# Kernel optimization log

Hardware: AMD Instinct MI355X
Metric: run time of the kernel (lower is better)

## Reference

```python
import jax, jax.numpy as jnp
import numpy as np
from jax import lax

C, K, EMB = 10, 32, 32
B, H, W = 32, 128, 128
DIRS = ((-1, 0), (1, 0), (0, -1), (0, 1))  # up, down, left, right


def _shift(x, dh, dw):
    # shift (B,H,W,...) by (dh,dw) with zero fill; x[b,h,w] <- x[b,h+dh,w+dw]
    pad = [(0, 0), (max(dh, 0), max(-dh, 0)), (max(dw, 0), max(-dw, 0))] + [(0, 0)] * (x.ndim - 3)
    xp = jnp.pad(x, pad)
    h0, w0 = max(-dh, 0), max(-dw, 0)
    return lax.dynamic_slice_in_dim(lax.dynamic_slice_in_dim(xp, h0, x.shape[1], 1), w0, x.shape[2], 2)


def conv(x, w, b):
    y = lax.conv_general_dilated(x, w, (1, 1), 'SAME',
                                 dimension_numbers=('NHWC', 'HWIO', 'NHWC'))
    return y + b


def small_cnn(x, w1, b1, w2, b2, w3, b3):
    x = jax.nn.relu(conv(x, w1, b1))
    x = jax.nn.relu(conv(x, w2, b2))
    return conv(x, w3, b3)


def neighbor_affinity(phi, tau=0.5):
    # phi: (B,H,W,D) -> w: (B,H,W,4) Gaussian feature affinity to 4 neighbors
    ones = jnp.ones(phi.shape[:3] + (1,), phi.dtype)
    ws = []
    for dh, dw in DIRS:
        nb = _shift(phi, dh, dw)
        valid = _shift(ones, dh, dw)[..., 0]
        d2 = jnp.sum((phi - nb) ** 2, axis=-1)
        ws.append(jnp.exp(-d2 / tau) * valid)
    return jnp.stack(ws, axis=-1)


def init_seeds_soft(Bv, Hv, Wv, Kv, dtype=jnp.float32):
    # K seeds on a gh x gw grid; soft assignment by squared distance
    gh = 4
    gw = Kv // gh
    sh = (jnp.arange(gh, dtype=dtype) + 0.5) * (Hv / gh)
    sw = (jnp.arange(gw, dtype=dtype) + 0.5) * (Wv / gw)
    seed_h = jnp.repeat(sh, gw)  # (K,)
    seed_w = jnp.tile(sw, gh)    # (K,)
    hh = jnp.arange(Hv, dtype=dtype)[:, None, None]
    ww = jnp.arange(Wv, dtype=dtype)[None, :, None]
    d2 = (hh - seed_h) ** 2 + (ww - seed_w) ** 2  # (H,W,K)
    sigma2 = (Hv / gh) * (Wv / gw)
    A = jax.nn.softmax(-d2 / sigma2, axis=-1)
    return jnp.broadcast_to(A[None], (Bv, Hv, Wv, Kv))


def soft_message_pass(A, w, beta=2.0):
    # aggregate neighbor assignments weighted by affinity, renormalize over K
    agg = jnp.zeros_like(A)
    for d, (dh, dw) in enumerate(DIRS):
        agg = agg + w[..., d:d + 1] * _shift(A, dh, dw)
    return jax.nn.softmax(beta * agg, axis=-1)


def soft_pool_features(G, A):
    # G:(B,H,W,C), A:(B,H,W,K) -> T:(B,K,1+2+C+4)
    Bv, Hv, Wv, Cv = G.shape
    eps = 1e-6
    mass = jnp.sum(A, axis=(1, 2)) + eps                      # (B,K)
    hh = (jnp.arange(Hv, dtype=G.dtype) + 0.5) / Hv
    ww = (jnp.arange(Wv, dtype=G.dtype) + 0.5) / Wv
    h_c = jnp.einsum('bhwk,h->bk', A, hh) / mass
    w_c = jnp.einsum('bhwk,w->bk', A, ww) / mass
    col = jnp.einsum('bhwk,bhwc->bkc', A, G) / mass[..., None]
    h2 = jnp.einsum('bhwk,h->bk', A, hh ** 2) / mass
    w2 = jnp.einsum('bhwk,w->bk', A, ww ** 2) / mass
    h_sd = jnp.sqrt(jax.nn.relu(h2 - h_c ** 2) + eps)
    w_sd = jnp.sqrt(jax.nn.relu(w2 - w_c ** 2) + eps)
    size = (mass / (Hv * Wv))[..., None]                      # (B,K,1)
    cen = jnp.stack([h_c, w_c], axis=-1)                      # (B,K,2)
    bbox = jnp.stack([h_c - h_sd, h_c + h_sd, w_c - w_sd, w_c + w_sd], axis=-1)
    return jnp.concatenate([size, cen, col, bbox], axis=-1)


def setup_inputs() -> dict:
    key = jax.random.key(0)
    ks = jax.random.split(key, 4)
    X = jax.random.randint(ks[0], (B, H, W), 0, C)
    w1 = jax.random.normal(ks[1], (3, 3, C, 32), jnp.float32) * (1.0 / np.sqrt(9 * C))
    w2 = jax.random.normal(ks[2], (3, 3, 32, 32), jnp.float32) * (1.0 / np.sqrt(9 * 32))
    w3 = jax.random.normal(ks[3], (1, 1, 32, EMB), jnp.float32) * (1.0 / np.sqrt(32))
    return {'X': X, 'w1': w1, 'b1': jnp.zeros((32,), jnp.float32),
            'w2': w2, 'b2': jnp.zeros((32,), jnp.float32),
            'w3': w3, 'b3': jnp.zeros((EMB,), jnp.float32)}


def reference(X, w1, b1, w2, b2, w3, b3):
    G = jax.nn.one_hot(X, C, dtype=jnp.float32)              # (B,H,W,C)
    phi = small_cnn(G, w1, b1, w2, b2, w3, b3)               # (B,H,W,EMB)
    w = neighbor_affinity(phi)                               # (B,H,W,4)
    A = init_seeds_soft(G.shape[0], G.shape[1], G.shape[2], K, G.dtype)
    for _ in range(8):
        A = soft_message_pass(A, w, beta=2.0)
    T = soft_pool_features(G, A)
    return A, T
```

## Files before the change

### kernel.cpp

```cpp
#include <hip/hip_runtime.h>
#include <math.h>

#define HD 128
#define WD 128
#define BB 32
#define KK 32
#define NPIX (BB*HD*WD)

typedef _Float16 f16;
typedef __attribute__((ext_vector_type(8))) _Float16 f16x8;
typedef __attribute__((ext_vector_type(4))) float f32x4;

__device__ __forceinline__ int swz(int row, int g){
  return row*64 + (((g + (row >> 1)) & 3) << 4);
}

__global__ __launch_bounds__(512, 2) void cnn_kernel(
    const int* __restrict__ X,
    const float* __restrict__ w1, const float* __restrict__ b1,
    const float* __restrict__ w2, const float* __restrict__ b2,
    const float* __restrict__ w3, const float* __restrict__ b3,
    f16* __restrict__ phi)
{
  __shared__ f16 sW1f[9*11*40];
  __shared__ int   sX[20*36];
  __shared__ float sB2[32], sB3[32];
  __shared__ f16 x1[612*32];
  __shared__ f16 w2t[9*32*32];
  __shared__ f16 w3t[32*32];

  const int tid = threadIdx.x;
  const int img = blockIdx.z;
  const int bh0 = blockIdx.y * 16;
  const int bw0 = blockIdx.x * 32;

  for (int i = tid; i < 9*11*32; i += 512) {
    int tap = i / 352, c = (i % 352) >> 5, oc = i & 31;
    float v = (c < 10) ? w1[tap*320 + c*32 + oc] : 0.f;
    if (tap == 4 && c < 10) v += b1[oc];
    sW1f[(tap*11 + c)*40 + oc] = (f16)v;
  }
  for (int i = tid; i < 9*32*32; i += 512) {
    int tap = i >> 10, ic = (i >> 5) & 31, oc = i & 31;
    int off = swz(tap*32 + oc, ic >> 3) + (ic & 7)*2;
    *(f16*)((char*)w2t + off) = (f16)w2[i];
  }
  for (int i = tid; i < 32*32; i += 512) {
    int ic = i >> 5, oe = i & 31;
    int off = swz(oe, ic >> 3) + (ic & 7)*2;
    *(f16*)((char*)w3t + off) = (f16)w3[i];
  }
  if (tid < 32) { sB2[tid] = b2[tid]; sB3[tid] = b3[tid]; }
  for (int i = tid; i < 20*36; i += 512) {
    int ti = i / 36, tj = i % 36;
    int gh = bh0 - 2 + ti, gw = bw0 - 2 + tj;
    sX[i] = (gh >= 0 && gh < HD && gw >= 0 && gw < WD) ? X[(img*HD + gh)*WD + gw] : 10;
  }
  __syncthreads();

  for (int p = tid; p < 612; p += 512) {
    int hr = p / 34, hc = p - hr*34;
    int gh = bh0 + hr - 1, gw = bw0 + hc - 1;
    if (gh >= 0 && gh < HD && gw >= 0 && gw < WD) {
      f16x8 acc[4];
      {
        int c = sX[hr*36 + hc];
        const f16* wr = &sW1f[c*40];
        #pragma unroll
        for (int g = 0; g < 4; g++) acc[g] = *(const f16x8*)(wr + g*8);
      }
      #pragma unroll
      for (int tap = 1; tap < 9; tap++) {
        const int ti = tap/3, tj = tap%3;
        int c = sX[(hr+ti)*36 + hc + tj];
        const f16* wr = &sW1f[(tap*11 + c)*40];
        #pragma unroll
        for (int g = 0; g < 4; g++) acc[g] += *(const f16x8*)(wr + g*8);
      }
      f16x8 z;
      #pragma unroll
      for (int j = 0; j < 8; j++) z[j] = (f16)0.f;
      #pragma unroll
      for (int g = 0; g < 4; g++) {
        f16x8 r = acc[g];
        #pragma unroll
        for (int j = 0; j < 8; j++) r[j] = (r[j] > (f16)0.f) ? r[j] : (f16)0.f;
        *(f16x8*)((char*)x1 + swz(p, g)) = r;
      }
    } else {
      f16x8 z;
      #pragma unroll
      for (int j = 0; j < 8; j++) z[j] = (f16)0.f;
      #pragma unroll
      for (int g = 0; g < 4; g++) *(f16x8*)((char*)x1 + swz(p, g)) = z;
    }
  }
  __syncthreads();

  const int lane = tid & 63;
  const int wv   = tid >> 6;
  const int lr   = lane & 15;
  const int kg   = lane >> 4;
  const int mts  = wv * 4;

  int arow0[4];
  #pragma unroll
  for (int q = 0; q < 4; q++) {
    int px = (mts + q)*16 + lr;
    arow0[q] = (px >> 5)*34 + (px & 31);
  }
  float b2v0 = sB2[lr], b2v1 = sB2[lr + 16];
  f32x4 acc[4][2];
  #pragma unroll
  for (int q = 0; q < 4; q++) {
    acc[q][0] = (f32x4){b2v0, b2v0, b2v0, b2v0};
    acc[q][1] = (f32x4){b2v1, b2v1, b2v1, b2v1};
  }
  #pragma unroll
  for (int tap = 0; tap < 9; tap++) {
    const int ti = tap/3, tj = tap%3;
    f16x8 bf0 = *(const f16x8*)((const char*)w2t + swz(tap*32 + lr,      kg));
    f16x8 bf1 = *(const f16x8*)((const char*)w2t + swz(tap*32 + lr + 16, kg));
    #pragma unroll
    for (int q = 0; q < 4; q++) {
      int row = arow0[q] + ti*34 + tj;
      f16x8 af = *(const f16x8*)((const char*)x1 + swz(row, kg));
      acc[q][0] = __builtin_amdgcn_mfma_f32_16x16x32_f16(af, bf0, acc[q][0], 0, 0, 0);
      acc[q][1] = __builtin_amdgcn_mfma_f32_16x16x32_f16(af, bf1, acc[q][1], 0, 0, 0);
    }
  }
  __syncthreads();

  #pragma unroll
  for (int q = 0; q < 4; q++)
    #pragma unroll
    for (int nt = 0; nt < 2; nt++) {
      int oc = nt*16 + lr;
      #pragma unroll
      for (int rg = 0; rg < 4; rg++) {
        int px = (mts + q)*16 + kg*4 + rg;
        int off = swz(px, oc >> 3) + (oc & 7)*2;
        *(f16*)((char*)x1 + off) = (f16)fmaxf(acc[q][nt][rg], 0.f);
      }
    }
  __syncthreads();

  {
    f16x8 cf0 = *(const f16x8*)((const char*)w3t + swz(lr,      kg));
    f16x8 cf1 = *(const f16x8*)((const char*)w3t + swz(lr + 16, kg));
    float b3v0 = sB3[lr], b3v1 = sB3[lr + 16];
    #pragma unroll
    for (int q = 0; q < 4; q++) {
      f16x8 af = *(const f16x8*)((const char*)x1 + swz((mts + q)*16 + lr, kg));
      f32x4 o0 = (f32x4){b3v0, b3v0, b3v0, b3v0};
      f32x4 o1 = (f32x4){b3v1, b3v1, b3v1, b3v1};
      o0 = __builtin_amdgcn_mfma_f32_16x16x32_f16(af, cf0, o0, 0, 0, 0);
      o1 = __builtin_amdgcn_mfma_f32_16x16x32_f16(af, cf1, o1, 0, 0, 0);
      #pragma unroll
      for (int rg = 0; rg < 4; rg++) {
        int px = (mts + q)*16 + kg*4 + rg;
        int gh = bh0 + (px >> 5), gw = bw0 + (px & 31);
        f16* dst = phi + ((size_t)((img*HD + gh)*WD + gw))*32;
        dst[lr]      = (f16)o0[rg];
        dst[lr + 16] = (f16)o1[rg];
      }
    }
  }
}

__device__ __forceinline__ float aff_one(const f16x8* __restrict__ nb,
                                         f16x8 c0, f16x8 c1, f16x8 c2, f16x8 c3,
                                         bool valid) {
  if (!valid) return 0.f;
  f16x8 d0 = c0 - nb[0]; f16x8 s = d0*d0;
  f16x8 d1 = c1 - nb[1]; s += d1*d1;
  f16x8 d2 = c2 - nb[2]; s += d2*d2;
  f16x8 d3 = c3 - nb[3]; s += d3*d3;
  float d2f = 0.f;
  #pragma unroll
  for (int j = 0; j < 8; j++) d2f += (float)s[j];
  return __expf(-2.f * d2f);
}

__global__ __launch_bounds__(256) void aff_kernel(const f16* __restrict__ phi, float* __restrict__ wb) {
  const int t = blockIdx.x * 256 + threadIdx.x;
  const int w = t & (WD-1), h = (t >> 7) & (HD-1);
  const f16x8* pc = (const f16x8*)(phi + (size_t)t * 32);
  f16x8 c0 = pc[0], c1 = pc[1], c2 = pc[2], c3 = pc[3];
  float4 out;
  out.x = aff_one(pc + WD*4, c0,c1,c2,c3, h < HD-1);
  out.y = aff_one(pc - WD*4, c0,c1,c2,c3, h > 0);
  out.z = aff_one(pc + 4,    c0,c1,c2,c3, w < WD-1);
  out.w = aff_one(pc - 4,    c0,c1,c2,c3, w > 0);
  ((float4*)wb)[t] = out;
}

__device__ __forceinline__ void a0_accum(float* a, int hh, int ww, float wt) {
  const float fh = (float)hh, fw = (float)ww;
  float e[32]; float s = 0.f;
  #pragma unroll
  for (int kh = 0; kh < 4; kh++) {
    float dh = fh - (float)(kh*32 + 16);
    float dh2 = dh*dh;
    #pragma unroll
    for (int kw = 0; kw < 8; kw++) {
      float dw = fw - (float)(kw*16 + 8);
      float x = __expf(-(dh2 + dw*dw) * (1.f/512.f));
      e[kh*8+kw] = x; s += x;
    }
  }
  float sc = wt / s;
  #pragma unroll
  for (int k = 0; k < 32; k++) a[k] = fmaf(e[k], sc, a[k]);
}

template<int FIRST, int LAST>
__global__ __launch_bounds__(256, 4) void mp2_kernel(const f16* __restrict__ Ain,
                                                     const float* __restrict__ wb,
                                                     f16* __restrict__ Aout,
                                                     float* __restrict__ AoutF) {
  __shared__ f16 amid[612*32];

  const int blk  = blockIdx.x;
  const int cxcd = blk & 7;
  const int q    = blk >> 3;
  const int tile = q & 31;
  const int img  = cxcd + ((q >> 5) << 3);
  const int th0  = (tile >> 2) * 16;
  const int tw0  = (tile & 3) * 32;
  const size_t ibase = (size_t)img * HD * WD;

  for (int p = threadIdx.x; p < 612; p += 256) {
    int r = p / 34, cc = p - r*34;
    int gh = th0 - 1 + r, gw = tw0 - 1 + cc;
    bool inimg = (gh >= 0 && gh < HD && gw >= 0 && gw < WD);
    int ghc = min(max(gh, 0), HD-1), gwc = min(max(gw, 0), WD-1);
    float4 wd = make_float4(0.f, 0.f, 0.f, 0.f);
    if (inimg) wd = ((const float4*)wb)[ibase + gh*WD + gw];

    int hu = (ghc < HD-1) ? ghc+1 : ghc;
    int hd = (ghc > 0)    ? ghc-1 : ghc;
    int wl = (gwc < WD-1) ? gwc+1 : gwc;
    int wr = (gwc > 0)    ? gwc-1 : gwc;

    float a[32];
    #pragma unroll
    for (int k = 0; k < 32; k++) a[k] = 0.f;

    if (FIRST) {
      a0_accum(a, hu, gwc, wd.x);
      a0_accum(a, hd, gwc, wd.y);
      a0_accum(a, ghc, wl, wd.z);
      a0_accum(a, ghc, wr, wd.w);
    } else {
      f16x8 agg[4];
      #pragma unroll
      for (int g = 0; g < 4; g++)
        #pragma unroll
        for (int j = 0; j < 8; j++) agg[g][j] = (f16)0.f;
      const size_t i0 = ibase + (size_t)hu*WD + gwc;
      const size_t i1 = ibase + (size_t)hd*WD + gwc;
      const size_t i2 = ibase + (size_t)ghc*WD + wl;
      const size_t i3 = ibase + (size_t)ghc*WD + wr;
      const f16x8* s0 = (const f16x8*)(Ain + i0*32);
      const f16x8* s1 = (const f16x8*)(Ain + i1*32);
      const f16x8* s2 = (const f16x8*)(Ain + i2*32);
      const f16x8* s3 = (const f16x8*)(Ain + i3*32);
      f16 w0 = (f16)wd.x, w1 = (f16)wd.y, w2 = (f16)wd.z, w3 = (f16)wd.w;
      #pragma unroll
      for (int g = 0; g < 4; g++) {
        f16x8 v0 = s0[g], v1 = s1[g], v2 = s2[g], v3 = s3[g];
        #pragma unroll
        for (int j = 0; j < 8; j++)
          agg[g][j] = v0[j]*w0 + v1[j]*w1 + v2[j]*w2 + v3[j]*w3;
      }
      #pragma unroll
      for (int g = 0; g < 4; g++)
        #pragma unroll
        for (int j = 0; j < 8; j++) a[g*8+j] = (float)agg[g][j];
    }

    float s = 0.f;
    #pragma unroll
    for (int k = 0; k < 32; k++) { a[k] = __expf(a[k] + a[k]); s += a[k]; }
    float inv = 1.f / s;
    #pragma unroll
    for (int g = 0; g < 4; g++) {
      f16x8 o;
      #pragma unroll
      for (int j = 0; j < 8; j++) o[j] = (f16)(a[g*8+j] * inv);
      *(f16x8*)((char*)amid + swz(p, g)) = o;
    }
  }
  __syncthreads();

  for (int p = threadIdx.x; p < 512; p += 256) {
    int r2 = p >> 5, c2 = p & 31;
    int gh = th0 + r2, gw = tw0 + c2;
    int rm = r2 + 1, cm = c2 + 1;
    float4 wd = ((const float4*)wb)[ibase + gh*WD + gw];

    int ru = rm + ((gh < HD-1) ? 1 : 0);
    int rd = rm - ((gh > 0)    ? 1 : 0);
    int cl = cm + ((gw < WD-1) ? 1 : 0);
    int cr = cm - ((gw > 0)    ? 1 : 0);
    int p0 = ru*34 + cm, p1 = rd*34 + cm, p2 = rm*34 + cl, p3 = rm*34 + cr;

    f16 w0 = (f16)wd.x, w1 = (f16)wd.y, w2 = (f16)wd.z, w3 = (f16)wd.w;
    float a[32];
    #pragma unroll
    for (int g = 0; g < 4; g++) {
      f16x8 v0 = *(const f16x8*)((const char*)amid + swz(p0, g));
      f16x8 v1 = *(const f16x8*)((const char*)amid + swz(p1, g));
      f16x8 v2 = *(const f16x8*)((const char*)amid + swz(p2, g));
      f16x8 v3 = *(const f16x8*)((const char*)amid + swz(p3, g));
      #pragma unroll
      for (int j = 0; j < 8; j++) {
        f16 x = v0[j]*w0 + v1[j]*w1 + v2[j]*w2 + v3[j]*w3;
        a[g*8+j] = (float)x;
      }
    }
    float s = 0.f;
    #pragma unroll
    for (int k = 0; k < 32; k++) { a[k] = __expf(a[k] + a[k]); s += a[k]; }
    float inv = 1.f / s;
    size_t opix = ibase + (size_t)gh*WD + gw;
    if (LAST) {
      float4* dst = (float4*)(AoutF + opix*32);
      #pragma unroll
      for (int g = 0; g < 8; g++)
        dst[g] = make_float4(a[4*g]*inv, a[4*g+1]*inv, a[4*g+2]*inv, a[4*g+3]*inv);
    } else {
      f16x8* dst = (f16x8*)(Aout + opix*32);
      #pragma unroll
      for (int g = 0; g < 4; g++) {
        f16x8 o;
        #pragma unroll
        for (int j = 0; j < 8; j++) o[j] = (f16)(a[g*8+j]*inv);
        dst[g] = o;
      }
    }
  }
}

__global__ __launch_bounds__(256) void pool1_kernel(const float* __restrict__ A,
                                                    const int* __restrict__ X,
                                                    float* __restrict__ part) {
  const int b = blockIdx.x, cy = blockIdx.y;
  const int k = threadIdx.x & 31, sub = threadIdx.x >> 5;
  const int h = cy*4 + (sub >> 1);
  const int w0 = (sub & 1) * 64;
  const float hh = ((float)h + 0.5f) * (1.f/128.f);
  float s0 = 0.f, sw = 0.f, sw2 = 0.f;
  float col[10];
  #pragma unroll
  for (int c = 0; c < 10; c++) col[c] = 0.f;
  const float* Arow = A + ((size_t)((b*HD + h)*WD + w0))*32 + k;
  const int*   Xrow = X + (b*HD + h)*WD + w0;
  for (int w = 0; w < 64; w++) {
    float a  = Arow[(size_t)w*32];
    float ww = ((float)(w + w0) + 0.5f) * (1.f/128.f);
    s0 += a; sw = fmaf(ww, a, sw); sw2 = fmaf(ww*ww, a, sw2);
    int x = Xrow[w];
    #pragma unroll
    for (int c = 0; c < 10; c++) col[c] += (x == c) ? a : 0.f;
  }
  __shared__ float red[8][32][15];
  float vals[15];
  vals[0] = s0; vals[1] = hh*s0; vals[2] = sw; vals[3] = hh*hh*s0; vals[4] = sw2;
  #pragma unroll
  for (int c = 0; c < 10; c++) vals[5+c] = col[c];
  #pragma unroll
  for (int q = 0; q < 15; q++) red[sub][k][q] = vals[q];
  __syncthreads();
  if (sub == 0) {
    #pragma unroll
    for (int q = 0; q < 15; q++) {
      float v = 0.f;
      #pragma unroll
      for (int s2 = 0; s2 < 8; s2++) v += red[s2][k][q];
      part[(((size_t)b*32 + cy)*32 + k)*15 + q] = v;
    }
  }
}

__global__ __launch_bounds__(256) void pool2_kernel(const float* __restrict__ part,
                                                    float* __restrict__ T) {
  const int t = blockIdx.x * 256 + threadIdx.x;
  if (t >= BB*KK) return;
  const int b = t >> 5, k = t & 31;
  float s[15];
  #pragma unroll
  for (int q = 0; q < 15; q++) s[q] = 0.f;
  for (int cy = 0; cy < 32; cy++) {
    const float* p = part + (((size_t)b*32 + cy)*32 + k)*15;
    #pragma unroll
    for (int q = 0; q < 15; q++) s[q] += p[q];
  }
  float mass = s[0] + 1e-6f;
  float inv  = 1.f / mass;
  float h_c = s[1]*inv, w_c = s[2]*inv, h2 = s[3]*inv, w2 = s[4]*inv;
  float h_sd = sqrtf(fmaxf(h2 - h_c*h_c, 0.f) + 1e-6f);
  float w_sd = sqrtf(fmaxf(w2 - w_c*w_c, 0.f) + 1e-6f);
  float* o = T + (size_t)t*17;
  o[0] = mass * (1.f/16384.f);
  o[1] = h_c; o[2] = w_c;
  #pragma unroll
  for (int c = 0; c < 10; c++) o[3+c] = s[5+c]*inv;
  o[13] = h_c - h_sd; o[14] = h_c + h_sd; o[15] = w_c - w_sd; o[16] = w_c + w_sd;
}

extern "C" void kernel_launch(void* const* d_in, const int* in_sizes, int n_in,
                              void* d_out, int out_size, void* d_ws, size_t ws_size,
                              hipStream_t stream) {
  const int*   X  = (const int*)d_in[0];
  const float* w1 = (const float*)d_in[1];
  const float* b1 = (const float*)d_in[2];
  const float* w2 = (const float*)d_in[3];
  const float* b2 = (const float*)d_in[4];
  const float* w3 = (const float*)d_in[5];
  const float* b3 = (const float*)d_in[6];

  float* out   = (float*)d_out;
  float* A_out = out;
  float* T_out = out + (size_t)NPIX * KK;

  char*  ws   = (char*)d_ws;
  f16*   bufA = (f16*)ws;
  float* wb   = (float*)(ws + (size_t)32*1024*1024);
  f16*   bufB = (f16*)(ws + (size_t)40*1024*1024);
  float* part = (float*)ws;

  f16* phi = bufB;
  cnn_kernel<<<dim3(WD/32, HD/16, BB), 512, 0, stream>>>(X, w1, b1, w2, b2, w3, b3, phi);
  aff_kernel<<<NPIX/256, 256, 0, stream>>>(phi, wb);

  mp2_kernel<1,0><<<1024, 256, 0, stream>>>(nullptr, wb, bufA, nullptr);
  mp2_kernel<0,0><<<1024, 256, 0, stream>>>(bufA, wb, bufB, nullptr);
  mp2_kernel<0,0><<<1024, 256, 0, stream>>>(bufB, wb, bufA, nullptr);
  mp2_kernel<0,1><<<1024, 256, 0, stream>>>(bufA, wb, nullptr, A_out);

  pool1_kernel<<<dim3(BB, 32), 256, 0, stream>>>(A_out, X, part);
  pool2_kernel<<<(BB*KK + 255)/256, 256, 0, stream>>>(part, T_out);
}
```

Before: 287.7 us.

## Stage halo tiles in LDS for affinity and message-pass kernels

The affinity kernel now loads a 16x32 tile plus a one-pixel halo of phi into shared memory and reads the neighbours from there, replacing four global gathers per pixel. The non-first message-pass kernels preload a 2-pixel halo of A (36x20) into a larger shared buffer, compute the intermediate step from LDS, hold the results in registers and then overwrite the buffer. This cuts redundant global reads, but the larger LDS footprint lowers occupancy (launch bounds go from 4 to 3 blocks) and adds extra barriers.

```diff
diff --git a/kernel.cpp b/kernel.cpp
--- a/kernel.cpp
+++ b/kernel.cpp
@@ -77,9 +77,6 @@
         #pragma unroll
         for (int g = 0; g < 4; g++) acc[g] += *(const f16x8*)(wr + g*8);
       }
-      f16x8 z;
-      #pragma unroll
-      for (int j = 0; j < 8; j++) z[j] = (f16)0.f;
       #pragma unroll
       for (int g = 0; g < 4; g++) {
         f16x8 r = acc[g];
@@ -168,31 +165,58 @@
   }
 }
 
-__device__ __forceinline__ float aff_one(const f16x8* __restrict__ nb,
+__device__ __forceinline__ float aff_lds(const f16* __restrict__ sphi, int slot,
                                          f16x8 c0, f16x8 c1, f16x8 c2, f16x8 c3,
                                          bool valid) {
-  if (!valid) return 0.f;
-  f16x8 d0 = c0 - nb[0]; f16x8 s = d0*d0;
-  f16x8 d1 = c1 - nb[1]; s += d1*d1;
-  f16x8 d2 = c2 - nb[2]; s += d2*d2;
-  f16x8 d3 = c3 - nb[3]; s += d3*d3;
+  f16x8 n0 = *(const f16x8*)((const char*)sphi + swz(slot, 0));
+  f16x8 n1 = *(const f16x8*)((const char*)sphi + swz(slot, 1));
+  f16x8 n2 = *(const f16x8*)((const char*)sphi + swz(slot, 2));
+  f16x8 n3 = *(const f16x8*)((const char*)sphi + swz(slot, 3));
+  f16x8 d0 = c0 - n0; f16x8 s = d0*d0;
+  f16x8 d1 = c1 - n1; s += d1*d1;
+  f16x8 d2 = c2 - n2; s += d2*d2;
+  f16x8 d3 = c3 - n3; s += d3*d3;
   float d2f = 0.f;
   #pragma unroll
   for (int j = 0; j < 8; j++) d2f += (float)s[j];
-  return __expf(-2.f * d2f);
-}
-
-__global__ __launch_bounds__(256) void aff_kernel(const f16* __restrict__ phi, float* __restrict__ wb) {
-  const int t = blockIdx.x * 256 + threadIdx.x;
-  const int w = t & (WD-1), h = (t >> 7) & (HD-1);
-  const f16x8* pc = (const f16x8*)(phi + (size_t)t * 32);
-  f16x8 c0 = pc[0], c1 = pc[1], c2 = pc[2], c3 = pc[3];
-  float4 out;
-  out.x = aff_one(pc + WD*4, c0,c1,c2,c3, h < HD-1);
-  out.y = aff_one(pc - WD*4, c0,c1,c2,c3, h > 0);
-  out.z = aff_one(pc + 4,    c0,c1,c2,c3, w < WD-1);
-  out.w = aff_one(pc - 4,    c0,c1,c2,c3, w > 0);
-  ((float4*)wb)[t] = out;
+  return valid ? __expf(-2.f * d2f) : 0.f;
+}
+
+__global__ __launch_bounds__(256, 4) void aff_kernel(const f16* __restrict__ phi, float* __restrict__ wb) {
+  __shared__ f16 sphi[612*32];
+
+  const int blk  = blockIdx.x;
+  const int tile = blk & 31;
+  const int img  = blk >> 5;
+  const int th0  = (tile >> 2) * 16;
+  const int tw0  = (tile & 3) * 32;
+  const size_t ibase = (size_t)img * HD * WD;
+
+  for (int task = threadIdx.x; task < 2448; task += 256) {
+    int p = task >> 2, g = task & 3;
+    int r = p / 34, c = p - r*34;
+    int gh = min(max(th0 - 1 + r, 0), HD-1);
+    int gw = min(max(tw0 - 1 + c, 0), WD-1);
+    f16x8 v = *(const f16x8*)(phi + (ibase + gh*WD + gw)*32 + g*8);
+    *(f16x8*)((char*)sphi + swz(p, g)) = v;
+  }
+  __syncthreads();
+
+  for (int p2 = threadIdx.x; p2 < 512; p2 += 256) {
+    int r2 = p2 >> 5, c2 = p2 & 31;
+    int gh = th0 + r2, gw = tw0 + c2;
+    int qc = (r2+1)*34 + (c2+1);
+    f16x8 c0 = *(const f16x8*)((const char*)sphi + swz(qc, 0));
+    f16x8 c1 = *(const f16x8*)((const char*)sphi + swz(qc, 1));
+    f16x8 c2v = *(const f16x8*)((const char*)sphi + swz(qc, 2));
+    f16x8 c3 = *(const f16x8*)((const char*)sphi + swz(qc, 3));
+    float4 out;
+    out.x = aff_lds(sphi, qc + 34, c0,c1,c2v,c3, gh < HD-1);
+    out.y = aff_lds(sphi, qc - 34, c0,c1,c2v,c3, gh > 0);
+    out.z = aff_lds(sphi, qc + 1,  c0,c1,c2v,c3, gw < WD-1);
+    out.w = aff_lds(sphi, qc - 1,  c0,c1,c2v,c3, gw > 0);
+    ((float4*)wb)[ibase + gh*WD + gw] = out;
+  }
 }
 
 __device__ __forceinline__ void a0_accum(float* a, int hh, int ww, float wt) {
@@ -215,11 +239,11 @@
 }
 
 template<int FIRST, int LAST>
-__global__ __launch_bounds__(256, 4) void mp2_kernel(const f16* __restrict__ Ain,
+__global__ __launch_bounds__(256, 3) void mp2_kernel(const f16* __restrict__ Ain,
                                                      const float* __restrict__ wb,
                                                      f16* __restrict__ Aout,
                                                      float* __restrict__ AoutF) {
-  __shared__ f16 amid[612*32];
+  __shared__ f16 buf[720*32];
 
   const int blk  = blockIdx.x;
   const int cxcd = blk & 7;
@@ -230,10 +254,26 @@
   const int tw0  = (tile & 3) * 32;
   const size_t ibase = (size_t)img * HD * WD;
 
-  for (int p = threadIdx.x; p < 612; p += 256) {
+  if (!FIRST) {
+    for (int task = threadIdx.x; task < 2880; task += 256) {
+      int p = task >> 2, g = task & 3;
+      int r = p / 36, c = p - r*36;
+      int gh = min(max(th0 - 2 + r, 0), HD-1);
+      int gw = min(max(tw0 - 2 + c, 0), WD-1);
+      f16x8 v = *(const f16x8*)(Ain + (ibase + gh*WD + gw)*32 + g*8);
+      *(f16x8*)((char*)buf + swz(p, g)) = v;
+    }
+    __syncthreads();
+  }
+
+  f16x8 res[3][4];
+  #pragma unroll
+  for (int it = 0; it < 3; it++) {
+    int p = threadIdx.x + it*256;
+    if (p >= 612) continue;
     int r = p / 34, cc = p - r*34;
     int gh = th0 - 1 + r, gw = tw0 - 1 + cc;
-    bool inimg = (gh >= 0 && gh < HD && gw >= 0 && gw < WD);
+    bool inimg = ((unsigned)gh < (unsigned)HD) && ((unsigned)gw < (unsigned)WD);
     int ghc = min(max(gh, 0), HD-1), gwc = min(max(gw, 0), WD-1);
     float4 wd = make_float4(0.f, 0.f, 0.f, 0.f);
     if (inimg) wd = ((const float4*)wb)[ibase + gh*WD + gw];
@@ -253,31 +293,23 @@
       a0_accum(a, ghc, wl, wd.z);
       a0_accum(a, ghc, wr, wd.w);
     } else {
-      f16x8 agg[4];
-      #pragma unroll
-      for (int g = 0; g < 4; g++)
+      int su = (hu - th0 + 2)*36 + (gwc - tw0 + 2);
+      int sd = (hd - th0 + 2)*36 + (gwc - tw0 + 2);
+      int sl = (ghc - th0 + 2)*36 + (wl - tw0 + 2);
+      int sr = (ghc - th0 + 2)*36 + (wr - tw0 + 2);
+      f16 w0 = (f16)wd.x, w1 = (f16)wd.y, w2 = (f16)wd.z, w3 = (f16)wd.w;
+      #pragma unroll
+      for (int g = 0; g < 4; g++) {
+        f16x8 v0 = *(const f16x8*)((const char*)buf + swz(su, g));
+        f16x8 v1 = *(const f16x8*)((const char*)buf + swz(sd, g));
+        f16x8 v2 = *(const f16x8*)((const char*)buf + swz(sl, g));
+        f16x8 v3 = *(const f16x8*)((const char*)buf + swz(sr, g));
         #pragma unroll
-        for (int j = 0; j < 8; j++) agg[g][j] = (f16)0.f;
-      const size_t i0 = ibase + (size_t)hu*WD + gwc;
-      const size_t i1 = ibase + (size_t)hd*WD + gwc;
-      const size_t i2 = ibase + (size_t)ghc*WD + wl;
-      const size_t i3 = ibase + (size_t)ghc*WD + wr;
-      const f16x8* s0 = (const f16x8*)(Ain + i0*32);
-      const f16x8* s1 = (const f16x8*)(Ain + i1*32);
-      const f16x8* s2 = (const f16x8*)(Ain + i2*32);
-      const f16x8* s3 = (const f16x8*)(Ain + i3*32);
-      f16 w0 = (f16)wd.x, w1 = (f16)wd.y, w2 = (f16)wd.z, w3 = (f16)wd.w;
-      #pragma unroll
-      for (int g = 0; g < 4; g++) {
-        f16x8 v0 = s0[g], v1 = s1[g], v2 = s2[g], v3 = s3[g];
-        #pragma unroll
-        for (int j = 0; j < 8; j++)
-          agg[g][j] = v0[j]*w0 + v1[j]*w1 + v2[j]*w2 + v3[j]*w3;
-      }
-      #pragma unroll
-      for (int g = 0; g < 4; g++)
-        #pragma unroll
-        for (int j = 0; j < 8; j++) a[g*8+j] = (float)agg[g][j];
+        for (int j = 0; j < 8; j++) {
+          f16 x = v0[j]*w0 + v1[j]*w1 + v2[j]*w2 + v3[j]*w3;
+          a[g*8+j] = (float)x;
+        }
+      }
     }
 
     float s = 0.f;
@@ -289,31 +321,40 @@
       f16x8 o;
       #pragma unroll
       for (int j = 0; j < 8; j++) o[j] = (f16)(a[g*8+j] * inv);
-      *(f16x8*)((char*)amid + swz(p, g)) = o;
-    }
-  }
-  __syncthreads();
-
-  for (int p = threadIdx.x; p < 512; p += 256) {
-    int r2 = p >> 5, c2 = p & 31;
+      res[it][g] = o;
+    }
+  }
+  __syncthreads();
+
+  #pragma unroll
+  for (int it = 0; it < 3; it++) {
+    int p = threadIdx.x + it*256;
+    if (p >= 612) continue;
+    #pragma unroll
+    for (int g = 0; g < 4; g++)
+      *(f16x8*)((char*)buf + swz(p, g)) = res[it][g];
+  }
+  __syncthreads();
+
+  for (int p2 = threadIdx.x; p2 < 512; p2 += 256) {
+    int r2 = p2 >> 5, c2 = p2 & 31;
     int gh = th0 + r2, gw = tw0 + c2;
     int rm = r2 + 1, cm = c2 + 1;
     float4 wd = ((const float4*)wb)[ibase + gh*WD + gw];
 
-    int ru = rm + ((gh < HD-1) ? 1 : 0);
-    int rd = rm - ((gh > 0)    ? 1 : 0);
-    int cl = cm + ((gw < WD-1) ? 1 : 0);
-    int cr = cm - ((gw > 0)    ? 1 : 0);
-    int p0 = ru*34 + cm, p1 = rd*34 + cm, p2 = rm*34 + cl, p3 = rm*34 + cr;
+    int q0 = (rm + ((gh < HD-1) ? 1 : 0))*34 + cm;
+    int q1 = (rm - ((gh > 0)    ? 1 : 0))*34 + cm;
+    int q2 = rm*34 + cm + ((gw < WD-1) ? 1 : 0);
+    int q3 = rm*34 + cm - ((gw > 0)    ? 1 : 0);
 
     f16 w0 = (f16)wd.x, w1 = (f16)wd.y, w2 = (f16)wd.z, w3 = (f16)wd.w;
     float a[32];
     #pragma unroll
     for (int g = 0; g < 4; g++) {
-      f16x8 v0 = *(const f16x8*)((const char*)amid + swz(p0, g));
-      f16x8 v1 = *(const f16x8*)((const char*)amid + swz(p1, g));
-      f16x8 v2 = *(const f16x8*)((const char*)amid + swz(p2, g));
-      f16x8 v3 = *(const f16x8*)((const char*)amid + swz(p3, g));
+      f16x8 v0 = *(const f16x8*)((const char*)buf + swz(q0, g));
+      f16x8 v1 = *(const f16x8*)((const char*)buf + swz(q1, g));
+      f16x8 v2 = *(const f16x8*)((const char*)buf + swz(q2, g));
+      f16x8 v3 = *(const f16x8*)((const char*)buf + swz(q3, g));
       #pragma unroll
       for (int j = 0; j < 8; j++) {
         f16 x = v0[j]*w0 + v1[j]*w1 + v2[j]*w2 + v3[j]*w3;
@@ -433,7 +474,7 @@
 
   f16* phi = bufB;
   cnn_kernel<<<dim3(WD/32, HD/16, BB), 512, 0, stream>>>(X, w1, b1, w2, b2, w3, b3, phi);
-  aff_kernel<<<NPIX/256, 256, 0, stream>>>(phi, wb);
+  aff_kernel<<<1024, 256, 0, stream>>>(phi, wb);
 
   mp2_kernel<1,0><<<1024, 256, 0, stream>>>(nullptr, wb, bufA, nullptr);
   mp2_kernel<0,0><<<1024, 256, 0, stream>>>(bufA, wb, bufB, nullptr);
```

New measurement: 307.5 us. +6.9%, slower.
